# Performance work log

Measured on AMD Instinct MI355X. Metric: run time of the kernel, lower is better.

Reference implementation:

```python
import jax, jax.numpy as jnp
import numpy as np

N_EX, N_KC, D, HID, NHEADS = 10000, 500, 128, 128, 2
B, S = 256, 500
ALPHA = 0.2
NEG = -9e15


def setup_inputs() -> dict:
    key = jax.random.key(0)
    ks = jax.random.split(key, 24)
    sc = 0.1
    inp = {
        "adj_exercise_kc": jax.random.randint(ks[0], (N_EX, N_KC), 0, 2, dtype=jnp.int32),
        "kc_data": jax.random.randint(ks[1], (B, S), 0, N_KC).astype(jnp.int64),
        "exercise_data": jax.random.randint(ks[2], (B, S), 0, N_EX + 1).astype(jnp.int64),
        "exercise_respond_data": jax.random.randint(ks[3], (B, S), 0, 2 * N_EX + 1).astype(jnp.int64),
        "target": jax.random.randint(ks[4], (B * (S - 1), 1), 0, 2).astype(jnp.float32),
        # learned parameters
        "ex_embed": jax.random.normal(ks[5], (N_EX, D)) * sc,
        "kc_embed": jax.random.normal(ks[6], (N_KC, D)) * sc,
        "W1": jax.random.normal(ks[7], (NHEADS, D, D)) * sc,        # per-head shared proj
        "a_att": jax.random.normal(ks[8], (NHEADS, 2 * D, 1)) * sc,  # attention vector
        "E": jax.random.normal(ks[9], (NHEADS, D, D)) * sc,
        "rd_w": jax.random.normal(ks[10], (NHEADS, D, 2 * D)) * sc,  # reduceDim (mode 3)
        "rd_b": jnp.zeros((NHEADS, D)),
        "w_ih": jax.random.normal(ks[11], (4 * HID, 2 * D)) * sc,
        "w_hh": jax.random.normal(ks[12], (4 * HID, HID)) * sc,
        "b_ih": jnp.zeros((4 * HID,)),
        "b_hh": jnp.zeros((4 * HID,)),
        "fc1_w": jax.random.normal(ks[13], (HID, D + HID)) * sc,
        "fc1_b": jnp.zeros((HID,)),
        "fc2_w": jax.random.normal(ks[14], (1, HID)) * sc,
        "fc2_b": jnp.zeros((1,)),
    }
    return inp


def _gat_head(ex_h, kc_h, adj, W1h, ah, Eh, rdw, rdb):
    # mode == 3 GAT head. a_input @ a decomposes: e[i,j] = LReLU(exWh[i].a1 + kcWh[j].a2)
    kc_Wh = kc_h @ W1h                                   # [Nkc, D]
    ex_Wh = ex_h @ W1h                                   # [Nex, D]
    e = jax.nn.leaky_relu(ex_Wh @ ah[:D] + (kc_Wh @ ah[D:]).T, ALPHA)  # [Nex, Nkc]
    att = jax.nn.softmax(jnp.where(adj > 0, e, NEG), axis=1)
    new_kc = att @ kc_Wh                                 # [Nex, D]
    ex_Eh = ex_h @ Eh
    emb = jnp.concatenate([new_kc, new_kc * ex_Eh], axis=1) @ rdw.T + rdb
    return jax.nn.elu(emb)                               # [Nex, D]


def _lstm(x, w_ih, w_hh, b_ih, b_hh):
    # single-layer torch LSTM, gate order i,f,g,o
    b = x.shape[0]
    xg = jnp.einsum('bsi,gi->sbg', x, w_ih) + b_ih + b_hh  # [S,B,4H]

    def step(carry, xt):
        h, c = carry
        g = xt + h @ w_hh.T
        i, f, gg, o = jnp.split(g, 4, axis=-1)
        c = jax.nn.sigmoid(f) * c + jax.nn.sigmoid(i) * jnp.tanh(gg)
        h = jax.nn.sigmoid(o) * jnp.tanh(c)
        return (h, c), h

    init = (jnp.zeros((b, HID), x.dtype), jnp.zeros((b, HID), x.dtype))
    _, hs = jax.lax.scan(step, init, xg)
    return jnp.swapaxes(hs, 0, 1)                        # [B,S,H]


def _forward(adj, exercise_data, respond_data, target,
             ex_embed, kc_embed, W1, a_att, E, rd_w, rd_b,
             w_ih, w_hh, b_ih, b_hh, fc1_w, fc1_b, fc2_w, fc2_b):
    heads = jax.vmap(_gat_head, in_axes=(None, None, None, 0, 0, 0, 0, 0))(
        ex_embed, kc_embed, adj, W1, a_att, E, rd_w, rd_b)   # [NH, Nex, D]
    # torch: cat(dim=1).view(Nex, D, NH).mean(2) -> interleaved reshape of the concat
    cat = jnp.swapaxes(heads, 0, 1).reshape(N_EX, NHEADS * D)
    exercise_embedding = cat.reshape(N_EX, D, NHEADS).mean(-1)  # [Nex, D]

    emb0 = jnp.concatenate([jnp.zeros((1, D), exercise_embedding.dtype), exercise_embedding], 0)
    assess = emb0[exercise_data]                          # [B,S,D]

    zeros = jnp.zeros_like(exercise_embedding)
    resp_emb = jnp.concatenate([
        jnp.concatenate([zeros, exercise_embedding], -1),
        jnp.concatenate([exercise_embedding, zeros], -1)], 0)  # [2Nex, 2D]
    resp0 = jnp.concatenate([jnp.zeros((1, 2 * D), resp_emb.dtype), resp_emb], 0)
    lstm_input = resp0[respond_data]                      # [B,S,2D]

    learn = _lstm(lstm_input, w_ih, w_hh, b_ih, b_hh)[:, :S - 1, :]  # [B,S-1,H]
    assess = assess[:, 1:, :]                             # [B,S-1,D]

    y = jax.nn.relu(jnp.concatenate([learn, assess], -1) @ fc1_w.T + fc1_b)
    pred = (y @ fc2_w.T + fc2_b).reshape(-1)              # [B*(S-1)]
    t = target.reshape(-1)                                # all targets >= 0 => mask all-true
    # BCE with logits, mean reduction
    loss = jnp.mean(jnp.maximum(pred, 0) - pred * t + jnp.log1p(jnp.exp(-jnp.abs(pred))))
    return loss, jax.nn.sigmoid(pred), t


def reference(adj_exercise_kc, kc_data, exercise_data, exercise_respond_data, target,
              ex_embed, kc_embed, W1, a_att, E, rd_w, rd_b,
              w_ih, w_hh, b_ih, b_hh, fc1_w, fc1_b, fc2_w, fc2_b):
    del kc_data  # unused by the original forward body
    return _forward(adj_exercise_kc, exercise_data, exercise_respond_data, target,
                    ex_embed, kc_embed, W1, a_att, E, rd_w, rd_b,
                    w_ih, w_hh, b_ih, b_hh, fc1_w, fc1_b, fc2_w, fc2_b)
```

## Files before the change

### kernel.cpp

```cpp
#include <hip/hip_runtime.h>
#include <math.h>

#define N_EX 10000
#define N_KC 500
#define D 128
#define HID 128
#define BB 256
#define SS 500
#define NROWS 127744

typedef float vf4 __attribute__((ext_vector_type(4)));
typedef _Float16 hf2 __attribute__((ext_vector_type(2)));

__device__ __forceinline__ float sigm(float x) { return 1.f / (1.f + __expf(-x)); }
__device__ __forceinline__ float tanh_fast(float x) { return 1.f - 2.f / (1.f + __expf(2.f * x)); }

__device__ __forceinline__ hf2 u2h(unsigned v) { union { unsigned u; hf2 h; } x; x.u = v; return x.h; }

__device__ __forceinline__ float quad_sum(float x) {
    int a = __builtin_amdgcn_update_dpp(0, __float_as_int(x), 0xB1, 0xF, 0xF, true);
    x += __int_as_float(a);
    int b = __builtin_amdgcn_update_dpp(0, __float_as_int(x), 0x4E, 0xF, 0xF, true);
    x += __int_as_float(b);
    return x;
}

__global__ void k_precomp(const float* rd_w, const float* w_ih, const float* fc1_w,
                          const float* b_ih, const float* b_hh, const float* W1, const float* a_att,
                          const float* w_hh,
                          float* rd_wT, float* w_ihT0, float* w_ihT1,
                          float* fc1_AT, float* fc1_BT, float* gbias4, float* v1,
                          unsigned short* wlstm16, float* projC) {
    int idx = blockIdx.x * blockDim.x + threadIdx.x;
    int stride = gridDim.x * blockDim.x;
    const int N1 = 2 * 256 * 128;
    const int N2 = 128 * 512;
    const int N3 = 128 * 512;
    const int N4 = 128 * 128;
    const int N5 = 128 * 128;
    const int N6 = 512;
    const int N7 = 256;
    const int N8 = 65536;
    int total = N1 + N2 + N3 + N4 + N5 + N6 + N7 + N8;
    for (int tt = idx; tt < total; tt += stride) {
        int u = tt;
        if (u < N1) {
            int h = u / (256 * 128); int rem = u % (256 * 128); int c = rem / 128; int dd = rem % 128;
            rd_wT[u] = rd_w[h * 128 * 256 + dd * 256 + c];
        } else if ((u -= N1) < N2) {
            int k = u / 512, g = u % 512; w_ihT0[u] = w_ih[g * 256 + k];
        } else if ((u -= N2) < N3) {
            int k = u / 512, g = u % 512; w_ihT1[u] = w_ih[g * 256 + 128 + k];
        } else if ((u -= N3) < N4) {
            int k = u / 128, j = u % 128; fc1_AT[u] = fc1_w[j * 256 + k];
        } else if ((u -= N4) < N5) {
            int k = u / 128, j = u % 128; fc1_BT[u] = fc1_w[j * 256 + 128 + k];
        } else if ((u -= N5) < N6) {
            int uu = u >> 2, g = u & 3;
            float v = b_ih[g * 128 + uu] + b_hh[g * 128 + uu];
            gbias4[u] = v;
            projC[u] = v;
        } else if ((u -= N6) < N7) {
            int h = u / 128, k = u % 128;
            const float* wr = W1 + h * 16384 + k * 128;
            const float* av = a_att + h * 256;
            float acc = 0.f;
            for (int d = 0; d < 128; ++d) acc += wr[d] * av[d];
            v1[u] = acc;
        } else {
            u -= N7;
            int x = u & 7;
            int t = (u >> 3) & 511;
            int i = u >> 12;
            int g = i >> 2, j = i & 3;
            int uu = t >> 2, q = t & 3;
            float val = w_hh[(g * 128 + uu) * 128 + q * 32 + j * 8 + x];
            ((_Float16*)wlstm16)[u] = (_Float16)val;
        }
    }
}

__global__ void k_kc(const float* kc_embed, const float* W1, const float* a_att,
                     float* kc_Wh, float* s_kc) {
    int j = blockIdx.x, h = blockIdx.y, d = threadIdx.x;
    __shared__ float row[128];
    __shared__ float red[128];
    row[d] = kc_embed[j * 128 + d];
    __syncthreads();
    const float* w = W1 + h * 16384;
    float acc = 0.f;
    for (int k = 0; k < 128; ++k) acc += row[k] * w[k * 128 + d];
    kc_Wh[(h * 500 + j) * 128 + d] = acc;
    red[d] = acc * a_att[h * 256 + 128 + d];
    __syncthreads();
    for (int s = 64; s > 0; s >>= 1) { if (d < s) red[d] += red[d + s]; __syncthreads(); }
    if (d == 0) s_kc[h * 500 + j] = red[0];
}

__global__ void k_sex(const float* ex_embed, const float* v1, float* s_ex) {
    int t = blockIdx.x * blockDim.x + threadIdx.x;
    if (t >= 2 * N_EX) return;
    int h = t / N_EX, i = t % N_EX;
    const float4* e4 = (const float4*)(ex_embed + (size_t)i * 128);
    const float4* v4 = (const float4*)(v1 + h * 128);
    float acc = 0.f;
    for (int k = 0; k < 32; ++k) {
        float4 a = e4[k], b = v4[k];
        acc += a.x * b.x + a.y * b.y + a.z * b.z + a.w * b.w;
    }
    s_ex[h * N_EX + i] = acc;
}

__global__ __launch_bounds__(256) void k_attnk(const int* adj, const float* s_ex, const float* s_kc,
                                               const float* kc_Wh, float* new_kc) {
    int i0 = blockIdx.x * 8, h = blockIdx.y, t = threadIdx.x;
    __shared__ float a_lds[8 * 500];
    __shared__ float skc_l[500];
    for (int j = t; j < 500; j += 256) skc_l[j] = s_kc[h * 500 + j];
    __syncthreads();
    {
        int lg = t >> 5, lane = t & 31;
        int i = i0 + lg;
        float sex = s_ex[h * N_EX + i];
        const int* arow = adj + (size_t)i * 500;
        float* arow_l = a_lds + lg * 500;
        float lmax = -INFINITY;
        for (int j = lane; j < 500; j += 32) {
            float e = sex + skc_l[j];
            e = (e >= 0.f) ? e : 0.2f * e;
            e = (arow[j] > 0) ? e : -INFINITY;
            arow_l[j] = e;
            lmax = fmaxf(lmax, e);
        }
#pragma unroll
        for (int m = 16; m > 0; m >>= 1) lmax = fmaxf(lmax, __shfl_xor(lmax, m));
        float lsum = 0.f;
        for (int j = lane; j < 500; j += 32) {
            float w = __expf(arow_l[j] - lmax);
            arow_l[j] = w;
            lsum += w;
        }
#pragma unroll
        for (int m = 16; m > 0; m >>= 1) lsum += __shfl_xor(lsum, m);
        float inv = 1.f / lsum;
        for (int j = lane; j < 500; j += 32) arow_l[j] *= inv;
    }
    __syncthreads();
    int d = t & 127, half = t >> 7;
    const float* kcw = kc_Wh + h * 500 * 128;
    float acc[4] = {0.f, 0.f, 0.f, 0.f};
    for (int j = 0; j < 500; ++j) {
        float w = kcw[j * 128 + d];
#pragma unroll
        for (int r = 0; r < 4; ++r) acc[r] += a_lds[(half * 4 + r) * 500 + j] * w;
    }
#pragma unroll
    for (int r = 0; r < 4; ++r)
        new_kc[((size_t)h * N_EX + i0 + half * 4 + r) * 128 + d] = acc[r];
}

__global__ void k_gat2(const float* new_kc, const float* ex_embed, const float* E,
                       const float* rd_wT, const float* rd_b, float* H) {
    int i0 = blockIdx.x * 8, h = blockIdx.y, t = threadIdx.x;
    int d = t & 127, half = t >> 7;
    __shared__ float exr[8 * 128], nk[8 * 128], pr[8 * 128];
    for (int idx = t; idx < 8 * 128; idx += 256) {
        exr[idx] = ex_embed[(size_t)i0 * 128 + idx];
        nk[idx]  = new_kc[((size_t)h * N_EX + i0) * 128 + idx];
    }
    __syncthreads();
    const float* Eh = E + h * 16384;
    float acc2[4] = {0.f, 0.f, 0.f, 0.f};
    for (int k = 0; k < 128; ++k) {
        float ev = Eh[k * 128 + d];
#pragma unroll
        for (int r = 0; r < 4; ++r) acc2[r] += exr[(half * 4 + r) * 128 + k] * ev;
    }
#pragma unroll
    for (int r = 0; r < 4; ++r) {
        int rr = half * 4 + r;
        pr[rr * 128 + d] = nk[rr * 128 + d] * acc2[r];
    }
    __syncthreads();
    const float* rt = rd_wT + h * 256 * 128;
    float acc3[4] = {0.f, 0.f, 0.f, 0.f};
    for (int c = 0; c < 128; ++c) {
        float w = rt[c * 128 + d];
#pragma unroll
        for (int r = 0; r < 4; ++r) acc3[r] += nk[(half * 4 + r) * 128 + c] * w;
    }
    for (int c = 0; c < 128; ++c) {
        float w = rt[(128 + c) * 128 + d];
#pragma unroll
        for (int r = 0; r < 4; ++r) acc3[r] += pr[(half * 4 + r) * 128 + c] * w;
    }
#pragma unroll
    for (int r = 0; r < 4; ++r) {
        int rr = half * 4 + r;
        float v = acc3[r] + rd_b[h * 128 + d];
        v = (v > 0.f) ? v : expm1f(v);
        H[((size_t)h * N_EX + i0 + rr) * 128 + d] = v;
    }
}

__global__ void k_merge(const float* H, float* emb_e) {
    int idx = blockIdx.x * blockDim.x + threadIdx.x;
    if (idx >= N_EX * 128) return;
    int i = idx >> 7, d = idx & 127;
    int hs = d >> 6;
    int c0 = (2 * d) & 127, c1 = (2 * d + 1) & 127;
    const float* row = H + ((size_t)hs * N_EX + i) * 128;
    emb_e[idx] = 0.5f * (row[c0] + row[c1]);
}

__global__ __launch_bounds__(512) void k_proj(const float* emb_e, const float* w_ihT0,
                                              const float* w_ihT1, const float* fc1_BT,
                                              const float* gbias4,
                                              float* projC, float* assessP) {
    int i0 = blockIdx.x * 16, g = threadIdx.x;
    int gate = g >> 7, uu = g & 127;
    int oidx = uu * 4 + gate;
    float gbl = gbias4[oidx];
    __shared__ float er[16 * 128];
    for (int idx = g; idx < 16 * 128; idx += 512) er[idx] = emb_e[(size_t)i0 * 128 + idx];
    __syncthreads();
    float a0[16], a1[16];
#pragma unroll
    for (int r = 0; r < 16; ++r) { a0[r] = 0.f; a1[r] = 0.f; }
    for (int k = 0; k < 128; ++k) {
        float w0 = w_ihT0[k * 512 + g], w1 = w_ihT1[k * 512 + g];
#pragma unroll
        for (int r = 0; r < 16; ++r) { float e = er[r * 128 + k]; a0[r] += e * w0; a1[r] += e * w1; }
    }
    for (int r = 0; r < 16; ++r) {
        projC[((size_t)(1 + i0 + r)) * 512 + oidx]        = a1[r] + gbl;
        projC[((size_t)(1 + N_EX + i0 + r)) * 512 + oidx] = a0[r] + gbl;
    }
    if (g < 128) {
        float b[16];
#pragma unroll
        for (int r = 0; r < 16; ++r) b[r] = 0.f;
        for (int k = 0; k < 128; ++k) {
            float w = fc1_BT[k * 128 + g];
#pragma unroll
            for (int r = 0; r < 16; ++r) b[r] += er[r * 128 + k] * w;
        }
        for (int r = 0; r < 16; ++r) assessP[((size_t)i0 + r) * 128 + g] = b[r];
    }
}

__global__ __launch_bounds__(512, 2) void k_lstm(const uint4* __restrict__ w16,
                                                 const float* __restrict__ projC,
                                                 const int* __restrict__ respond,
                                                 float* __restrict__ learn) {
    int b = blockIdx.x, t = threadIdx.x;
    int u = t >> 2, q = t & 3;
    __shared__ uint4 hbuf4[2][18];
    __shared__ int rrow[500];
    uint4 w[16];
#pragma unroll
    for (int i = 0; i < 16; ++i) w[i] = w16[i * 512 + t];
    for (int s = t; s < 500; s += 512) rrow[s] = respond[b * 500 + s];
    if (t < 36) ((unsigned*)hbuf4)[t * 4] = 0, ((unsigned*)hbuf4)[t * 4 + 1] = 0,
                ((unsigned*)hbuf4)[t * 4 + 2] = 0, ((unsigned*)hbuf4)[t * 4 + 3] = 0;
    float c = 0.f;
    __syncthreads();
    vf4 xg_n = ((const vf4*)(projC + (size_t)rrow[0] * 512))[u];
    for (int s = 0; s < 500; ++s) {
        int par = s & 1;
        vf4 xg = xg_n;
        if (s < 499) xg_n = ((const vf4*)(projC + (size_t)rrow[s + 1] * 512))[u];
        const uint4* hsegp = (const uint4*)((const unsigned short*)hbuf4[par] + q * 32);
        uint4 h4[4];
#pragma unroll
        for (int j = 0; j < 4; ++j) h4[j] = hsegp[j];
        float p0 = 0.f, p1 = 0.f, p2 = 0.f, p3 = 0.f;
#pragma unroll
        for (int j = 0; j < 4; ++j) {
            hf2 ha = u2h(h4[j].x), hb = u2h(h4[j].y), hc = u2h(h4[j].z), hd = u2h(h4[j].w);
            uint4 w0 = w[j], w1 = w[4 + j], w2 = w[8 + j], w3 = w[12 + j];
            p0 = __builtin_amdgcn_fdot2(u2h(w0.x), ha, p0, false);
            p0 = __builtin_amdgcn_fdot2(u2h(w0.y), hb, p0, false);
            p0 = __builtin_amdgcn_fdot2(u2h(w0.z), hc, p0, false);
            p0 = __builtin_amdgcn_fdot2(u2h(w0.w), hd, p0, false);
            p1 = __builtin_amdgcn_fdot2(u2h(w1.x), ha, p1, false);
            p1 = __builtin_amdgcn_fdot2(u2h(w1.y), hb, p1, false);
            p1 = __builtin_amdgcn_fdot2(u2h(w1.z), hc, p1, false);
            p1 = __builtin_amdgcn_fdot2(u2h(w1.w), hd, p1, false);
            p2 = __builtin_amdgcn_fdot2(u2h(w2.x), ha, p2, false);
            p2 = __builtin_amdgcn_fdot2(u2h(w2.y), hb, p2, false);
            p2 = __builtin_amdgcn_fdot2(u2h(w2.z), hc, p2, false);
            p2 = __builtin_amdgcn_fdot2(u2h(w2.w), hd, p2, false);
            p3 = __builtin_amdgcn_fdot2(u2h(w3.x), ha, p3, false);
            p3 = __builtin_amdgcn_fdot2(u2h(w3.y), hb, p3, false);
            p3 = __builtin_amdgcn_fdot2(u2h(w3.z), hc, p3, false);
            p3 = __builtin_amdgcn_fdot2(u2h(w3.w), hd, p3, false);
        }
        float gi = quad_sum(p0) + xg.x;
        float gf = quad_sum(p1) + xg.y;
        float gG = quad_sum(p2) + xg.z;
        float go = quad_sum(p3) + xg.w;
        float ii = sigm(gi), ff = sigm(gf), tg = tanh_fast(gG), oo = sigm(go);
        c = ff * c + ii * tg;
        float hh = oo * tanh_fast(c);
        if (q == 0) {
            union { unsigned short us; _Float16 hf; } cv; cv.hf = (_Float16)hh;
            ((unsigned short*)hbuf4[par ^ 1])[u] = cv.us;
            if (s < 499) learn[((size_t)b * 499 + s) * 128 + u] = hh;
        }
        __syncthreads();
    }
}

__global__ __launch_bounds__(256) void k_mlp(const float* __restrict__ learn,
                                             const float* __restrict__ assessP,
                                             const float* __restrict__ fc1_AT,
                                             const float* __restrict__ fc1_b,
                                             const float* __restrict__ fc2_w,
                                             const float* __restrict__ fc2_b,
                                             const int* __restrict__ exercise_data,
                                             const float* __restrict__ target,
                                             float* __restrict__ out,
                                             float* __restrict__ loss_accum) {
    int tile = blockIdx.x;
    int t = threadIdx.x;
    int jg = t & 31, rg = t >> 5;
    __shared__ float A_lds[64 * 128];
    __shared__ float x_lds[64 * 64];
    __shared__ float red[8];
    float4 acc[8];
#pragma unroll
    for (int r = 0; r < 8; ++r) acc[r] = make_float4(0.f, 0.f, 0.f, 0.f);
    int row0 = tile * 64;
    for (int kc = 0; kc < 2; ++kc) {
        for (int idx = t; idx < 64 * 128; idx += 256) A_lds[idx] = fc1_AT[kc * 64 * 128 + idx];
        for (int idx = t; idx < 64 * 64; idx += 256) {
            int r = idx >> 6, k = idx & 63;
            x_lds[idx] = learn[((size_t)row0 + r) * 128 + kc * 64 + k];
        }
        __syncthreads();
        const float4* A4 = (const float4*)A_lds;
        const float4* x4 = (const float4*)x_lds;
#pragma unroll 4
        for (int k4 = 0; k4 < 16; ++k4) {
            float4 av[4];
#pragma unroll
            for (int kk = 0; kk < 4; ++kk) av[kk] = A4[(k4 * 4 + kk) * 32 + jg];
#pragma unroll
            for (int r = 0; r < 8; ++r) {
                float4 xv = x4[(rg * 8 + r) * 16 + k4];
                acc[r].x += xv.x * av[0].x + xv.y * av[1].x + xv.z * av[2].x + xv.w * av[3].x;
                acc[r].y += xv.x * av[0].y + xv.y * av[1].y + xv.z * av[2].y + xv.w * av[3].y;
                acc[r].z += xv.x * av[0].z + xv.y * av[1].z + xv.z * av[2].z + xv.w * av[3].z;
                acc[r].w += xv.x * av[0].w + xv.y * av[1].w + xv.z * av[2].w + xv.w * av[3].w;
            }
        }
        __syncthreads();
    }
    int j = jg * 4;
    float4 b1 = *(const float4*)(fc1_b + j);
    float4 f2 = *(const float4*)(fc2_w + j);
    float fb2 = fc2_b[0];
    float lloss = 0.f;
#pragma unroll
    for (int r = 0; r < 8; ++r) {
        int n = row0 + rg * 8 + r;
        int b = n / 499;
        int sidx = n - b * 499;
        int e = exercise_data[b * 500 + sidx + 1];
        float4 aP = make_float4(0.f, 0.f, 0.f, 0.f);
        if (e > 0) aP = *(const float4*)(assessP + (size_t)(e - 1) * 128 + j);
        float y0 = acc[r].x + aP.x + b1.x; y0 = y0 > 0.f ? y0 : 0.f;
        float y1 = acc[r].y + aP.y + b1.y; y1 = y1 > 0.f ? y1 : 0.f;
        float y2 = acc[r].z + aP.z + b1.z; y2 = y2 > 0.f ? y2 : 0.f;
        float y3 = acc[r].w + aP.w + b1.w; y3 = y3 > 0.f ? y3 : 0.f;
        float s = y0 * f2.x + y1 * f2.y + y2 * f2.z + y3 * f2.w;
#pragma unroll
        for (int m = 16; m > 0; m >>= 1) s += __shfl_xor(s, m, 32);
        if (jg == 0) {
            float p = s + fb2;
            float tg = target[n];
            out[1 + n] = 1.f / (1.f + expf(-p));
            float ab = fabsf(p);
            lloss += fmaxf(p, 0.f) - p * tg + log1pf(expf(-ab));
            out[1 + NROWS + n] = tg;
        }
    }
    if (jg == 0) red[rg] = lloss;
    __syncthreads();
    if (t == 0) {
        float sum = 0.f;
#pragma unroll
        for (int g = 0; g < 8; ++g) sum += red[g];
        atomicAdd(loss_accum, sum);
    }
}

__global__ void k_final(const float* loss_accum, float* out) {
    out[0] = loss_accum[0] * (1.f / (float)NROWS);
}

extern "C" void kernel_launch(void* const* d_in, const int* in_sizes, int n_in,
                              void* d_out, int out_size, void* d_ws, size_t ws_size,
                              hipStream_t stream) {
    const int* adj            = (const int*)d_in[0];
    const int* exercise_data  = (const int*)d_in[2];
    const int* respond        = (const int*)d_in[3];
    const float* target       = (const float*)d_in[4];
    const float* ex_embed     = (const float*)d_in[5];
    const float* kc_embed     = (const float*)d_in[6];
    const float* W1           = (const float*)d_in[7];
    const float* a_att        = (const float*)d_in[8];
    const float* E            = (const float*)d_in[9];
    const float* rd_w         = (const float*)d_in[10];
    const float* rd_b         = (const float*)d_in[11];
    const float* w_ih         = (const float*)d_in[12];
    const float* w_hh         = (const float*)d_in[13];
    const float* b_ih         = (const float*)d_in[14];
    const float* b_hh         = (const float*)d_in[15];
    const float* fc1_w        = (const float*)d_in[16];
    const float* fc1_b        = (const float*)d_in[17];
    const float* fc2_w        = (const float*)d_in[18];
    const float* fc2_b        = (const float*)d_in[19];
    float* out = (float*)d_out;

    float* ws = (float*)d_ws;
    size_t off = 0;
    auto alloc = [&](size_t n) { float* p = ws + off; off += (n + 3) & ~(size_t)3; return p; };
    float* kc_Wh   = alloc(2 * 500 * 128);
    float* s_kc    = alloc(1000);
    float* v1      = alloc(256);
    float* s_ex    = alloc(2 * N_EX);
    float* H       = alloc((size_t)2 * N_EX * 128);
    float* emb_e   = alloc((size_t)N_EX * 128);
    float* rd_wT   = alloc(2 * 256 * 128);
    float* w_ihT0  = alloc(128 * 512);
    float* w_ihT1  = alloc(128 * 512);
    float* fc1_AT  = alloc(128 * 128);
    float* fc1_BT  = alloc(128 * 128);
    float* gbias4  = alloc(512);
    float* wlstm   = alloc(32768);
    float* new_kc  = alloc((size_t)2 * N_EX * 128);
    float* projC   = alloc((size_t)(2 * N_EX + 1) * 512);
    float* assessP = alloc((size_t)N_EX * 128);
    float* learn   = alloc((size_t)BB * 499 * 128);
    float* loss_accum = alloc(4);

    k_precomp<<<256, 256, 0, stream>>>(rd_w, w_ih, fc1_w, b_ih, b_hh, W1, a_att, w_hh,
                                       rd_wT, w_ihT0, w_ihT1, fc1_AT, fc1_BT, gbias4, v1,
                                       (unsigned short*)wlstm, projC);
    k_kc<<<dim3(500, 2), 128, 0, stream>>>(kc_embed, W1, a_att, kc_Wh, s_kc);
    k_sex<<<79, 256, 0, stream>>>(ex_embed, v1, s_ex);
    k_attnk<<<dim3(N_EX / 8, 2), 256, 0, stream>>>(adj, s_ex, s_kc, kc_Wh, new_kc);
    k_gat2<<<dim3(N_EX / 8, 2), 256, 0, stream>>>(new_kc, ex_embed, E, rd_wT, rd_b, H);
    k_merge<<<(N_EX * 128) / 256, 256, 0, stream>>>(H, emb_e);
    k_proj<<<N_EX / 16, 512, 0, stream>>>(emb_e, w_ihT0, w_ihT1, fc1_BT, gbias4, projC, assessP);
    hipMemsetAsync(loss_accum, 0, sizeof(float), stream);
    k_lstm<<<BB, 512, 0, stream>>>((const uint4*)wlstm, projC, respond, learn);
    k_mlp<<<NROWS / 64, 256, 0, stream>>>(learn, assessP, fc1_AT, fc1_b, fc2_w, fc2_b,
                                          exercise_data, target, out, loss_accum);
    k_final<<<1, 1, 0, stream>>>(loss_accum, out);
}
```

Measured before the change: 788.6 us.

## Stream LSTM recurrent weights from LDS and global instead of registers

The LSTM kernel no longer holds all 16 uint4 fp16 weight vectors per thread in registers. Seven slices are staged once into shared memory and the other nine are re-read from global memory (cache) on every timestep. This cuts register pressure, likely aiming for higher occupancy or fewer spills. In exchange each of the 500 sequential steps issues extra LDS and global loads on the critical recurrence path, adding latency per step.

```diff
diff --git a/kernel.cpp b/kernel.cpp
--- a/kernel.cpp
+++ b/kernel.cpp
@@ -255,17 +255,16 @@
                                                  float* __restrict__ learn) {
     int b = blockIdx.x, t = threadIdx.x;
     int u = t >> 2, q = t & 3;
+    __shared__ uint4 wlds[7 * 512];
     __shared__ uint4 hbuf4[2][18];
     __shared__ int rrow[500];
-    uint4 w[16];
-#pragma unroll
-    for (int i = 0; i < 16; ++i) w[i] = w16[i * 512 + t];
+    for (int i = t; i < 7 * 512; i += 512) wlds[i] = w16[i];
     for (int s = t; s < 500; s += 512) rrow[s] = respond[b * 500 + s];
-    if (t < 36) ((unsigned*)hbuf4)[t * 4] = 0, ((unsigned*)hbuf4)[t * 4 + 1] = 0,
-                ((unsigned*)hbuf4)[t * 4 + 2] = 0, ((unsigned*)hbuf4)[t * 4 + 3] = 0;
+    if (t < 36) { uint4 z = {0u, 0u, 0u, 0u}; ((uint4*)hbuf4)[t] = z; }
     float c = 0.f;
     __syncthreads();
     vf4 xg_n = ((const vf4*)(projC + (size_t)rrow[0] * 512))[u];
+    const uint4* gbase = w16 + 7 * 512 + t;
     for (int s = 0; s < 500; ++s) {
         int par = s & 1;
         vf4 xg = xg_n;
@@ -274,27 +273,36 @@
         uint4 h4[4];
 #pragma unroll
         for (int j = 0; j < 4; ++j) h4[j] = hsegp[j];
+        uint4 wg[9];
+#pragma unroll
+        for (int i = 0; i < 9; ++i) wg[i] = gbase[i * 512];
+        uint4 wl[7];
+#pragma unroll
+        for (int i = 0; i < 7; ++i) wl[i] = wlds[i * 512 + t];
+        uint4 W0[4] = {wl[0], wl[1], wl[2], wl[3]};
+        uint4 W1[4] = {wl[4], wl[5], wl[6], wg[0]};
+        uint4 W2[4] = {wg[1], wg[2], wg[3], wg[4]};
+        uint4 W3[4] = {wg[5], wg[6], wg[7], wg[8]};
         float p0 = 0.f, p1 = 0.f, p2 = 0.f, p3 = 0.f;
 #pragma unroll
         for (int j = 0; j < 4; ++j) {
             hf2 ha = u2h(h4[j].x), hb = u2h(h4[j].y), hc = u2h(h4[j].z), hd = u2h(h4[j].w);
-            uint4 w0 = w[j], w1 = w[4 + j], w2 = w[8 + j], w3 = w[12 + j];
-            p0 = __builtin_amdgcn_fdot2(u2h(w0.x), ha, p0, false);
-            p0 = __builtin_amdgcn_fdot2(u2h(w0.y), hb, p0, false);
-            p0 = __builtin_amdgcn_fdot2(u2h(w0.z), hc, p0, false);
-            p0 = __builtin_amdgcn_fdot2(u2h(w0.w), hd, p0, false);
-            p1 = __builtin_amdgcn_fdot2(u2h(w1.x), ha, p1, false);
-            p1 = __builtin_amdgcn_fdot2(u2h(w1.y), hb, p1, false);
-            p1 = __builtin_amdgcn_fdot2(u2h(w1.z), hc, p1, false);
-            p1 = __builtin_amdgcn_fdot2(u2h(w1.w), hd, p1, false);
-            p2 = __builtin_amdgcn_fdot2(u2h(w2.x), ha, p2, false);
-            p2 = __builtin_amdgcn_fdot2(u2h(w2.y), hb, p2, false);
-            p2 = __builtin_amdgcn_fdot2(u2h(w2.z), hc, p2, false);
-            p2 = __builtin_amdgcn_fdot2(u2h(w2.w), hd, p2, false);
-            p3 = __builtin_amdgcn_fdot2(u2h(w3.x), ha, p3, false);
-            p3 = __builtin_amdgcn_fdot2(u2h(w3.y), hb, p3, false);
-            p3 = __builtin_amdgcn_fdot2(u2h(w3.z), hc, p3, false);
-            p3 = __builtin_amdgcn_fdot2(u2h(w3.w), hd, p3, false);
+            p0 = __builtin_amdgcn_fdot2(u2h(W0[j].x), ha, p0, false);
+            p0 = __builtin_amdgcn_fdot2(u2h(W0[j].y), hb, p0, false);
+            p0 = __builtin_amdgcn_fdot2(u2h(W0[j].z), hc, p0, false);
+            p0 = __builtin_amdgcn_fdot2(u2h(W0[j].w), hd, p0, false);
+            p1 = __builtin_amdgcn_fdot2(u2h(W1[j].x), ha, p1, false);
+            p1 = __builtin_amdgcn_fdot2(u2h(W1[j].y), hb, p1, false);
+            p1 = __builtin_amdgcn_fdot2(u2h(W1[j].z), hc, p1, false);
+            p1 = __builtin_amdgcn_fdot2(u2h(W1[j].w), hd, p1, false);
+            p2 = __builtin_amdgcn_fdot2(u2h(W2[j].x), ha, p2, false);
+            p2 = __builtin_amdgcn_fdot2(u2h(W2[j].y), hb, p2, false);
+            p2 = __builtin_amdgcn_fdot2(u2h(W2[j].z), hc, p2, false);
+            p2 = __builtin_amdgcn_fdot2(u2h(W2[j].w), hd, p2, false);
+            p3 = __builtin_amdgcn_fdot2(u2h(W3[j].x), ha, p3, false);
+            p3 = __builtin_amdgcn_fdot2(u2h(W3[j].y), hb, p3, false);
+            p3 = __builtin_amdgcn_fdot2(u2h(W3[j].z), hc, p3, false);
+            p3 = __builtin_amdgcn_fdot2(u2h(W3[j].w), hd, p3, false);
         }
         float gi = quad_sum(p0) + xg.x;
         float gf = quad_sum(p1) + xg.y;
```

After: 819.5 us. 3.9% more time.

## Transpose GAT operands for vector LDS reads and store LSTM output in fp16

Applied to the files above, without the earlier changes.

kc_Wh is now stored transposed so each thread reads its attention weights in contiguous float4 chunks. The attention and GAT LDS buffers are laid out row-interleaved so four output rows come from one vector LDS load. The LSTM hidden-state output is written as fp16 and widened back to fp32 in the MLP kernel, halving that intermediate's memory traffic at some precision cost.

```diff
diff --git a/kernel.cpp b/kernel.cpp
--- a/kernel.cpp
+++ b/kernel.cpp
@@ -81,7 +81,7 @@
 }
 
 __global__ void k_kc(const float* kc_embed, const float* W1, const float* a_att,
-                     float* kc_Wh, float* s_kc) {
+                     float* kcWhT, float* s_kc) {
     int j = blockIdx.x, h = blockIdx.y, d = threadIdx.x;
     __shared__ float row[128];
     __shared__ float red[128];
@@ -90,7 +90,7 @@
     const float* w = W1 + h * 16384;
     float acc = 0.f;
     for (int k = 0; k < 128; ++k) acc += row[k] * w[k * 128 + d];
-    kc_Wh[(h * 500 + j) * 128 + d] = acc;
+    kcWhT[((size_t)(h * 128 + d)) * 500 + j] = acc;
     red[d] = acc * a_att[h * 256 + 128 + d];
     __syncthreads();
     for (int s = 64; s > 0; s >>= 1) { if (d < s) red[d] += red[d + s]; __syncthreads(); }
@@ -112,10 +112,11 @@
 }
 
 __global__ __launch_bounds__(256) void k_attnk(const int* adj, const float* s_ex, const float* s_kc,
-                                               const float* kc_Wh, float* new_kc) {
+                                               const float* kcWhT, float* new_kc) {
     int i0 = blockIdx.x * 8, h = blockIdx.y, t = threadIdx.x;
-    __shared__ float a_lds[8 * 500];
+    __shared__ vf4 at4[1500];
     __shared__ float skc_l[500];
+    float* at = (float*)at4;
     for (int j = t; j < 500; j += 256) skc_l[j] = s_kc[h * 500 + j];
     __syncthreads();
     {
@@ -123,83 +124,91 @@
         int i = i0 + lg;
         float sex = s_ex[h * N_EX + i];
         const int* arow = adj + (size_t)i * 500;
-        float* arow_l = a_lds + lg * 500;
         float lmax = -INFINITY;
         for (int j = lane; j < 500; j += 32) {
             float e = sex + skc_l[j];
             e = (e >= 0.f) ? e : 0.2f * e;
             e = (arow[j] > 0) ? e : -INFINITY;
-            arow_l[j] = e;
+            at[j * 12 + lg] = e;
             lmax = fmaxf(lmax, e);
         }
 #pragma unroll
         for (int m = 16; m > 0; m >>= 1) lmax = fmaxf(lmax, __shfl_xor(lmax, m));
         float lsum = 0.f;
         for (int j = lane; j < 500; j += 32) {
-            float w = __expf(arow_l[j] - lmax);
-            arow_l[j] = w;
+            float w = __expf(at[j * 12 + lg] - lmax);
+            at[j * 12 + lg] = w;
             lsum += w;
         }
 #pragma unroll
         for (int m = 16; m > 0; m >>= 1) lsum += __shfl_xor(lsum, m);
         float inv = 1.f / lsum;
-        for (int j = lane; j < 500; j += 32) arow_l[j] *= inv;
+        for (int j = lane; j < 500; j += 32) at[j * 12 + lg] *= inv;
     }
     __syncthreads();
     int d = t & 127, half = t >> 7;
-    const float* kcw = kc_Wh + h * 500 * 128;
-    float acc[4] = {0.f, 0.f, 0.f, 0.f};
-    for (int j = 0; j < 500; ++j) {
-        float w = kcw[j * 128 + d];
-#pragma unroll
-        for (int r = 0; r < 4; ++r) acc[r] += a_lds[(half * 4 + r) * 500 + j] * w;
-    }
-#pragma unroll
-    for (int r = 0; r < 4; ++r)
-        new_kc[((size_t)h * N_EX + i0 + half * 4 + r) * 128 + d] = acc[r];
-}
-
-__global__ void k_gat2(const float* new_kc, const float* ex_embed, const float* E,
-                       const float* rd_wT, const float* rd_b, float* H) {
+    const float* kcwd = kcWhT + ((size_t)(h * 128 + d)) * 500;
+    vf4 acc = {0.f, 0.f, 0.f, 0.f};
+    for (int j4 = 0; j4 < 125; ++j4) {
+        vf4 w = *(const vf4*)(kcwd + j4 * 4);
+        vf4 a0 = *(const vf4*)(at + (j4 * 4 + 0) * 12 + half * 4);
+        vf4 a1 = *(const vf4*)(at + (j4 * 4 + 1) * 12 + half * 4);
+        vf4 a2 = *(const vf4*)(at + (j4 * 4 + 2) * 12 + half * 4);
+        vf4 a3 = *(const vf4*)(at + (j4 * 4 + 3) * 12 + half * 4);
+        acc += a0 * w.x + a1 * w.y + a2 * w.z + a3 * w.w;
+    }
+    new_kc[((size_t)h * N_EX + i0 + half * 4 + 0) * 128 + d] = acc.x;
+    new_kc[((size_t)h * N_EX + i0 + half * 4 + 1) * 128 + d] = acc.y;
+    new_kc[((size_t)h * N_EX + i0 + half * 4 + 2) * 128 + d] = acc.z;
+    new_kc[((size_t)h * N_EX + i0 + half * 4 + 3) * 128 + d] = acc.w;
+}
+
+__global__ __launch_bounds__(256) void k_gat2(const float* new_kc, const float* ex_embed,
+                                              const float* E, const float* rd_wT,
+                                              const float* rd_b, float* H) {
     int i0 = blockIdx.x * 8, h = blockIdx.y, t = threadIdx.x;
     int d = t & 127, half = t >> 7;
-    __shared__ float exr[8 * 128], nk[8 * 128], pr[8 * 128];
+    __shared__ vf4 exrT4[256], nkT4[256], prT4[256];
+    float* exrT = (float*)exrT4;
+    float* nkT  = (float*)nkT4;
+    float* prT  = (float*)prT4;
     for (int idx = t; idx < 8 * 128; idx += 256) {
-        exr[idx] = ex_embed[(size_t)i0 * 128 + idx];
-        nk[idx]  = new_kc[((size_t)h * N_EX + i0) * 128 + idx];
+        int r = idx >> 7, k = idx & 127;
+        exrT[k * 8 + r] = ex_embed[(size_t)i0 * 128 + idx];
+        nkT[k * 8 + r]  = new_kc[((size_t)h * N_EX + i0) * 128 + idx];
     }
     __syncthreads();
     const float* Eh = E + h * 16384;
-    float acc2[4] = {0.f, 0.f, 0.f, 0.f};
+    vf4 acc2 = {0.f, 0.f, 0.f, 0.f};
     for (int k = 0; k < 128; ++k) {
         float ev = Eh[k * 128 + d];
-#pragma unroll
-        for (int r = 0; r < 4; ++r) acc2[r] += exr[(half * 4 + r) * 128 + k] * ev;
-    }
-#pragma unroll
-    for (int r = 0; r < 4; ++r) {
-        int rr = half * 4 + r;
-        pr[rr * 128 + d] = nk[rr * 128 + d] * acc2[r];
+        vf4 ex4 = *(const vf4*)(exrT + k * 8 + half * 4);
+        acc2 += ex4 * ev;
+    }
+    {
+        vf4 nk4 = *(const vf4*)(nkT + d * 8 + half * 4);
+        vf4 pr4 = nk4 * acc2;
+        *(vf4*)(prT + d * 8 + half * 4) = pr4;
     }
     __syncthreads();
     const float* rt = rd_wT + h * 256 * 128;
-    float acc3[4] = {0.f, 0.f, 0.f, 0.f};
+    vf4 acc3 = {0.f, 0.f, 0.f, 0.f};
     for (int c = 0; c < 128; ++c) {
         float w = rt[c * 128 + d];
-#pragma unroll
-        for (int r = 0; r < 4; ++r) acc3[r] += nk[(half * 4 + r) * 128 + c] * w;
+        vf4 nk4 = *(const vf4*)(nkT + c * 8 + half * 4);
+        acc3 += nk4 * w;
     }
     for (int c = 0; c < 128; ++c) {
         float w = rt[(128 + c) * 128 + d];
-#pragma unroll
-        for (int r = 0; r < 4; ++r) acc3[r] += pr[(half * 4 + r) * 128 + c] * w;
-    }
+        vf4 pr4 = *(const vf4*)(prT + c * 8 + half * 4);
+        acc3 += pr4 * w;
+    }
+    float rb = rd_b[h * 128 + d];
 #pragma unroll
     for (int r = 0; r < 4; ++r) {
-        int rr = half * 4 + r;
-        float v = acc3[r] + rd_b[h * 128 + d];
+        float v = ((r == 0) ? acc3.x : (r == 1) ? acc3.y : (r == 2) ? acc3.z : acc3.w) + rb;
         v = (v > 0.f) ? v : expm1f(v);
-        H[((size_t)h * N_EX + i0 + rr) * 128 + d] = v;
+        H[((size_t)h * N_EX + i0 + half * 4 + r) * 128 + d] = v;
     }
 }
 
@@ -252,7 +261,7 @@
 __global__ __launch_bounds__(512, 2) void k_lstm(const uint4* __restrict__ w16,
                                                  const float* __restrict__ projC,
                                                  const int* __restrict__ respond,
-                                                 float* __restrict__ learn) {
+                                                 unsigned short* __restrict__ learn16) {
     int b = blockIdx.x, t = threadIdx.x;
     int u = t >> 2, q = t & 3;
     __shared__ uint4 hbuf4[2][18];
@@ -261,8 +270,7 @@
 #pragma unroll
     for (int i = 0; i < 16; ++i) w[i] = w16[i * 512 + t];
     for (int s = t; s < 500; s += 512) rrow[s] = respond[b * 500 + s];
-    if (t < 36) ((unsigned*)hbuf4)[t * 4] = 0, ((unsigned*)hbuf4)[t * 4 + 1] = 0,
-                ((unsigned*)hbuf4)[t * 4 + 2] = 0, ((unsigned*)hbuf4)[t * 4 + 3] = 0;
+    if (t < 36) { uint4 z = {0u, 0u, 0u, 0u}; ((uint4*)hbuf4)[t] = z; }
     float c = 0.f;
     __syncthreads();
     vf4 xg_n = ((const vf4*)(projC + (size_t)rrow[0] * 512))[u];
@@ -306,13 +314,13 @@
         if (q == 0) {
             union { unsigned short us; _Float16 hf; } cv; cv.hf = (_Float16)hh;
             ((unsigned short*)hbuf4[par ^ 1])[u] = cv.us;
-            if (s < 499) learn[((size_t)b * 499 + s) * 128 + u] = hh;
+            if (s < 499) learn16[((size_t)b * 499 + s) * 128 + u] = cv.us;
         }
         __syncthreads();
     }
 }
 
-__global__ __launch_bounds__(256) void k_mlp(const float* __restrict__ learn,
+__global__ __launch_bounds__(256) void k_mlp(const unsigned short* __restrict__ learn16,
                                              const float* __restrict__ assessP,
                                              const float* __restrict__ fc1_AT,
                                              const float* __restrict__ fc1_b,
@@ -334,9 +342,12 @@
     int row0 = tile * 64;
     for (int kc = 0; kc < 2; ++kc) {
         for (int idx = t; idx < 64 * 128; idx += 256) A_lds[idx] = fc1_AT[kc * 64 * 128 + idx];
-        for (int idx = t; idx < 64 * 64; idx += 256) {
-            int r = idx >> 6, k = idx & 63;
-            x_lds[idx] = learn[((size_t)row0 + r) * 128 + kc * 64 + k];
+        for (int idx = t; idx < 64 * 32; idx += 256) {
+            int r = idx >> 5, k2 = idx & 31;
+            unsigned pv = *(const unsigned*)(learn16 + ((size_t)row0 + r) * 128 + kc * 64 + k2 * 2);
+            hf2 hp = u2h(pv);
+            x_lds[(r << 6) + k2 * 2]     = (float)hp.x;
+            x_lds[(r << 6) + k2 * 2 + 1] = (float)hp.y;
         }
         __syncthreads();
         const float4* A4 = (const float4*)A_lds;
@@ -427,7 +438,7 @@
     float* ws = (float*)d_ws;
     size_t off = 0;
     auto alloc = [&](size_t n) { float* p = ws + off; off += (n + 3) & ~(size_t)3; return p; };
-    float* kc_Wh   = alloc(2 * 500 * 128);
+    float* kcWhT   = alloc(2 * 128 * 500);
     float* s_kc    = alloc(1000);
     float* v1      = alloc(256);
     float* s_ex    = alloc(2 * N_EX);
@@ -443,21 +454,23 @@
     float* new_kc  = alloc((size_t)2 * N_EX * 128);
     float* projC   = alloc((size_t)(2 * N_EX + 1) * 512);
     float* assessP = alloc((size_t)N_EX * 128);
-    float* learn   = alloc((size_t)BB * 499 * 128);
+    float* learn16 = alloc((size_t)BB * 499 * 64);
     float* loss_accum = alloc(4);
 
     k_precomp<<<256, 256, 0, stream>>>(rd_w, w_ih, fc1_w, b_ih, b_hh, W1, a_att, w_hh,
                                        rd_wT, w_ihT0, w_ihT1, fc1_AT, fc1_BT, gbias4, v1,
                                        (unsigned short*)wlstm, projC);
-    k_kc<<<dim3(500, 2), 128, 0, stream>>>(kc_embed, W1, a_att, kc_Wh, s_kc);
+    k_kc<<<dim3(500, 2), 128, 0, stream>>>(kc_embed, W1, a_att, kcWhT, s_kc);
     k_sex<<<79, 256, 0, stream>>>(ex_embed, v1, s_ex);
-    k_attnk<<<dim3(N_EX / 8, 2), 256, 0, stream>>>(adj, s_ex, s_kc, kc_Wh, new_kc);
+    k_attnk<<<dim3(N_EX / 8, 2), 256, 0, stream>>>(adj, s_ex, s_kc, kcWhT, new_kc);
     k_gat2<<<dim3(N_EX / 8, 2), 256, 0, stream>>>(new_kc, ex_embed, E, rd_wT, rd_b, H);
     k_merge<<<(N_EX * 128) / 256, 256, 0, stream>>>(H, emb_e);
     k_proj<<<N_EX / 16, 512, 0, stream>>>(emb_e, w_ihT0, w_ihT1, fc1_BT, gbias4, projC, assessP);
     hipMemsetAsync(loss_accum, 0, sizeof(float), stream);
-    k_lstm<<<BB, 512, 0, stream>>>((const uint4*)wlstm, projC, respond, learn);
-    k_mlp<<<NROWS / 64, 256, 0, stream>>>(learn, assessP, fc1_AT, fc1_b, fc2_w, fc2_b,
+    k_lstm<<<BB, 512, 0, stream>>>((const uint4*)wlstm, projC, respond,
+                                   (unsigned short*)learn16);
+    k_mlp<<<NROWS / 64, 256, 0, stream>>>((const unsigned short*)learn16, assessP, fc1_AT,
+                                          fc1_b, fc2_w, fc2_b,
                                           exercise_data, target, out, loss_accum);
     k_final<<<1, 1, 0, stream>>>(loss_accum, out);
 }
```

Result: no change. 803.2 us (+1.8%).
